# Optimization experiments

Hardware: AMD Instinct MI355X
Metric: run time of the kernel (lower is better)

Reference implementation:

```python
import jax, jax.numpy as jnp
import numpy as np

N = 20000
E = 320000
BS = 1
FG = FN = FE = 128
H = 256


def _mlp_params(key, din, dout):
    dims = [(din, H), (H, H), (H, H), (H, dout)]
    ks = jax.random.split(key, 8)
    ws = [jax.random.normal(ks[2 * i], (a, b), jnp.float32) * (1.0 / np.sqrt(a).astype(np.float32)) for i, (a, b) in enumerate(dims)]
    bs = [jax.random.normal(ks[2 * i + 1], (b,), jnp.float32) * 0.01 for i, (a, b) in enumerate(dims)]
    return ws, bs


def setup_inputs() -> dict:
    key = jax.random.key(0)
    kg, kn, ke, ks, kr, kpe, kpn, kpg = jax.random.split(key, 8)
    inp = {
        'g': jax.random.normal(kg, (BS, FG), jnp.float32),
        'nodes': jax.random.normal(kn, (BS, N, FN), jnp.float32),
        'edges': jax.random.normal(ke, (BS, E, FE), jnp.float32),
        'senders': jax.random.randint(ks, (E,), 0, N, dtype=jnp.int32),
        'receivers': jax.random.randint(kr, (E,), 0, N, dtype=jnp.int32),
    }
    for prefix, kk, din, dout in [('e', kpe, FG + 2 * FN + FE, FE), ('n', kpn, FG + FN + FE, FN), ('g', kpg, FG + FN + FE, FG)]:
        ws, bs = _mlp_params(kk, din, dout)
        for i in range(4):
            inp[f'{prefix}w{i + 1}'] = ws[i]
            inp[f'{prefix}b{i + 1}'] = bs[i]
    return inp


def _mlp(x, w1, b1, w2, b2, w3, b3, w4, b4):
    h = jax.nn.relu(x @ w1 + b1)
    h = jax.nn.relu(h @ w2 + b2)
    h = jax.nn.relu(h @ w3 + b3)
    return h @ w4 + b4


def reference(g, nodes, edges, senders, receivers,
              ew1, eb1, ew2, eb2, ew3, eb3, ew4, eb4,
              nw1, nb1, nw2, nb2, nw3, nb3, nw4, nb4,
              gw1, gb1, gw2, gb2, gw3, gb3, gw4, gb4):
    bs, n_nodes, _ = nodes.shape
    n_edges = edges.shape[1]
    # edge update: concat(g, n_sender, n_receiver, e) -> 4-layer MLP
    g_e = jnp.broadcast_to(g[:, None, :], (bs, n_edges, g.shape[-1]))
    ns = nodes[:, senders]   # [bs, E, FN] gather
    nr = nodes[:, receivers]
    e_new = _mlp(jnp.concatenate([g_e, ns, nr, edges], axis=-1), ew1, eb1, ew2, eb2, ew3, eb3, ew4, eb4)
    # node update: sum of incoming (receiver-indexed) edge feats, scatter-add
    agg = jax.vmap(lambda e: jax.ops.segment_sum(e, receivers, num_segments=n_nodes))(e_new)  # [bs, N, FE]
    g_n = jnp.broadcast_to(g[:, None, :], (bs, n_nodes, g.shape[-1]))
    n_new = _mlp(jnp.concatenate([g_n, nodes, agg], axis=-1), nw1, nb1, nw2, nb2, nw3, nb3, nw4, nb4)
    # graph update: global sums of updated edge and node feats
    e_sum = e_new.sum(axis=1)  # [bs, FE]
    n_sum = n_new.sum(axis=1)  # [bs, FN]
    g_new = _mlp(jnp.concatenate([g, n_sum, e_sum], axis=-1), gw1, gb1, gw2, gb2, gw3, gb3, gw4, gb4)
    return e_new, n_new, g_new
```

## Files before the change

kernel.cpp:

```cpp
#include <hip/hip_runtime.h>
#include <stdint.h>

typedef __attribute__((ext_vector_type(8))) short bf16x8;
typedef __attribute__((ext_vector_type(4))) float f32x4;

#define NE 320000
#define NNODES 20000
#define SMEM_BYTES (65536 + 16384 + 32768)

__device__ __forceinline__ unsigned short f2bf(float f) {
  union { float f; unsigned int u; } v; v.f = f;
  unsigned int u = v.u;
  u += 0x7fffu + ((u >> 16) & 1u);
  return (unsigned short)(u >> 16);
}

__device__ __forceinline__ void gload_lds16(const void* g, void* l) {
  __builtin_amdgcn_global_load_lds((const __attribute__((address_space(1))) void*)g,
                                   (__attribute__((address_space(3))) void*)l, 16, 0, 0);
}

__device__ __forceinline__ void stage_b(const unsigned short* gsrc, char* lds, int nbytes,
                                        int w, int lane) {
  const char* gp = (const char*)gsrc + lane * 16;
  int niss = nbytes >> 10;
#pragma unroll
  for (int i = 0; i < 4; ++i) {
    int idx = w + i * 8;
    if (idx < niss) gload_lds16(gp + (idx << 10), lds + (idx << 10));
  }
}

struct PackArgs {
  const float* src[8];
  unsigned short* dst[8];
  int K[8];
  int N[8];
};

__global__ void pack_weights(PackArgs a) {
  int m = blockIdx.y;
  int K = a.K[m], N = a.N[m];
  int total = (K >> 3) * N;
  int idx = blockIdx.x * 256 + threadIdx.x;
  if (idx >= total) return;
  int n = idx % N;
  int kg = idx / N;
  const float* s = a.src[m];
  bf16x8 p;
#pragma unroll
  for (int j = 0; j < 8; ++j)
    p[j] = (short)f2bf(s[(size_t)(kg * 8 + j) * N + n]);
  *(bf16x8*)(a.dst[m] + (size_t)idx * 8) = p;
}

template <int NB>
__device__ __forceinline__ void compute_chunk(const char* Ab, int rowstride, int kbyte0,
                                              const char* Bb, int NN, int colbase,
                                              int wm, int lhi, int llo, f32x4 (&acc)[2][8]) {
#pragma unroll
  for (int ks = 0; ks < 2; ++ks) {
    bf16x8 a[2];
#pragma unroll
    for (int m = 0; m < 2; ++m) {
      int row = wm * 32 + m * 16 + llo;
      int off = (row * rowstride + kbyte0 + ks * 64 + lhi * 16) ^ ((row & 7) << 4);
      a[m] = *(const bf16x8*)(Ab + off);
    }
    bf16x8 b[NB];
#pragma unroll
    for (int n = 0; n < NB; ++n) {
      int off = ((ks * 4 + lhi) * NN + colbase + n * 16 + llo) * 16;
      b[n] = *(const bf16x8*)(Bb + off);
    }
#pragma unroll
    for (int m = 0; m < 2; ++m)
#pragma unroll
      for (int n = 0; n < NB; ++n)
        acc[m][n] = __builtin_amdgcn_mfma_f32_16x16x32_bf16(a[m], b[n], acc[m][n], 0, 0, 0);
  }
}

__device__ __forceinline__ void zero_acc(f32x4 (&acc)[2][8]) {
  f32x4 z = {0.f, 0.f, 0.f, 0.f};
#pragma unroll
  for (int m = 0; m < 2; ++m)
#pragma unroll
    for (int n = 0; n < 8; ++n) acc[m][n] = z;
}

__device__ __forceinline__ void write_h(char* Hb, const f32x4 (&acc)[2][8], const float* bias,
                                        int wm, int wn, int lhi, int llo) {
#pragma unroll
  for (int n = 0; n < 8; ++n) {
    int col = wn * 128 + n * 16 + llo;
    float bv = bias[col];
#pragma unroll
    for (int m = 0; m < 2; ++m)
#pragma unroll
      for (int q = 0; q < 4; ++q) {
        int row = wm * 32 + m * 16 + lhi * 4 + q;
        float v = fmaxf(acc[m][n][q] + bv, 0.0f);
        int off = (row * 512 + col * 2) ^ ((row & 7) << 4);
        *(unsigned short*)(Hb + off) = f2bf(v);
      }
  }
}

template <int MODE>
__global__ __launch_bounds__(512, 2) void fused_mlp(
    const float* __restrict__ gvec, const float* __restrict__ nodes,
    const float* __restrict__ third, const int* __restrict__ senders,
    const int* __restrict__ receivers,
    const unsigned short* __restrict__ pw1, const unsigned short* __restrict__ pw2,
    const unsigned short* __restrict__ pw3, const unsigned short* __restrict__ pw4,
    const float* __restrict__ b1, const float* __restrict__ b2,
    const float* __restrict__ b3, const float* __restrict__ b4,
    float* __restrict__ outp, float* __restrict__ aggp, float* __restrict__ colsum) {
  constexpr int K1 = (MODE == 0) ? 512 : 384;
  constexpr int KC1 = K1 / 64;
  constexpr int NROWS = (MODE == 0) ? NE : NNODES;

  extern __shared__ char smem[];
  char* Hb = smem;
  char* Ab = smem + 65536;
  char* Bb = smem + 81920;

  const int tid = threadIdx.x;
  const int lane = tid & 63;
  const int w = tid >> 6;
  const int wm = w & 3, wn = w >> 2;
  const int lhi = lane >> 4, llo = lane & 15;
  const int row0 = blockIdx.x * 128;

  const int grow = tid >> 2;
  const int qq = tid & 3;
  const float* src0 = gvec;
  const float* src1;
  const float* src2;
  const float* src3;
  if (MODE == 0) {
    int e = row0 + grow;
    src1 = nodes + (size_t)senders[e] * 128;
    src2 = nodes + (size_t)receivers[e] * 128;
    src3 = third + (size_t)e * 128;
  } else {
    int i = row0 + grow;
    bool v = i < NROWS;
    src1 = v ? nodes + (size_t)i * 128 : gvec;
    src2 = v ? third + (size_t)i * 128 : gvec;
    src3 = gvec;
  }

  f32x4 acc[2][8];
  zero_acc(acc);

  for (int c = 0; c < KC1; ++c) {
    {
      int gc = c * 64 + qq * 16;
      int region = gc >> 7;
      const float* sp = (region == 0) ? src0 : (region == 1) ? src1 : (region == 2) ? src2 : src3;
      sp += (gc & 127);
      f32x4 v0 = *(const f32x4*)(sp);
      f32x4 v1 = *(const f32x4*)(sp + 4);
      f32x4 v2 = *(const f32x4*)(sp + 8);
      f32x4 v3 = *(const f32x4*)(sp + 12);
      bf16x8 p0, p1;
#pragma unroll
      for (int j = 0; j < 4; ++j) {
        p0[j] = (short)f2bf(v0[j]);
        p0[4 + j] = (short)f2bf(v1[j]);
        p1[j] = (short)f2bf(v2[j]);
        p1[4 + j] = (short)f2bf(v3[j]);
      }
      int ab = grow * 128 + qq * 32;
      int sw = (grow & 7) << 4;
      *(bf16x8*)(Ab + (ab ^ sw)) = p0;
      *(bf16x8*)(Ab + ((ab + 16) ^ sw)) = p1;
    }
    stage_b(pw1 + (size_t)c * 16384, Bb, 32768, w, lane);
    __syncthreads();
    compute_chunk<8>(Ab, 128, 0, Bb, 256, wn * 128, wm, lhi, llo, acc);
    __syncthreads();
  }
  write_h(Hb, acc, b1, wm, wn, lhi, llo);
  __syncthreads();

  zero_acc(acc);
  for (int c = 0; c < 4; ++c) {
    stage_b(pw2 + (size_t)c * 16384, Bb, 32768, w, lane);
    __syncthreads();
    compute_chunk<8>(Hb, 512, c * 128, Bb, 256, wn * 128, wm, lhi, llo, acc);
    __syncthreads();
  }
  write_h(Hb, acc, b2, wm, wn, lhi, llo);
  __syncthreads();

  zero_acc(acc);
  for (int c = 0; c < 4; ++c) {
    stage_b(pw3 + (size_t)c * 16384, Bb, 32768, w, lane);
    __syncthreads();
    compute_chunk<8>(Hb, 512, c * 128, Bb, 256, wn * 128, wm, lhi, llo, acc);
    __syncthreads();
  }
  write_h(Hb, acc, b3, wm, wn, lhi, llo);
  __syncthreads();

  zero_acc(acc);
  for (int c = 0; c < 4; ++c) {
    stage_b(pw4 + (size_t)c * 8192, Bb, 16384, w, lane);
    __syncthreads();
    compute_chunk<4>(Hb, 512, c * 128, Bb, 128, wn * 64, wm, lhi, llo, acc);
    __syncthreads();
  }

  float cs[4] = {0.f, 0.f, 0.f, 0.f};
#pragma unroll
  for (int n = 0; n < 4; ++n) {
    int col = wn * 64 + n * 16 + llo;
    float bv = b4[col];
#pragma unroll
    for (int m = 0; m < 2; ++m)
#pragma unroll
      for (int q = 0; q < 4; ++q) {
        int gr = row0 + wm * 32 + m * 16 + lhi * 4 + q;
        float v = acc[m][n][q] + bv;
        if (MODE == 0) {
          outp[(size_t)gr * 128 + col] = v;
          atomicAdd(aggp + (size_t)receivers[gr] * 128 + col, v);
          cs[n] += v;
        } else {
          if (gr < NROWS) {
            outp[(size_t)gr * 128 + col] = v;
            cs[n] += v;
          }
        }
      }
  }
#pragma unroll
  for (int n = 0; n < 4; ++n) {
    float v = cs[n];
    v += __shfl_xor(v, 16);
    v += __shfl_xor(v, 32);
    if (lane < 16) atomicAdd(colsum + wn * 64 + n * 16 + llo, v);
  }
}

__global__ void global_mlp(const float* __restrict__ g, const float* __restrict__ nsum,
                           const float* __restrict__ esum, const float* __restrict__ w1,
                           const float* __restrict__ bb1, const float* __restrict__ w2,
                           const float* __restrict__ bb2, const float* __restrict__ w3,
                           const float* __restrict__ bb3, const float* __restrict__ w4,
                           const float* __restrict__ bb4, float* __restrict__ outg) {
  __shared__ float x[384], h1[256], h2[256], h3[256];
  int t = threadIdx.x;
  if (t < 128) x[t] = g[t];
  else if (t < 256) x[t] = nsum[t - 128];
  else x[t] = esum[t - 256];
  __syncthreads();
  if (t < 256) {
    float a = bb1[t];
    for (int k = 0; k < 384; ++k) a = fmaf(x[k], w1[k * 256 + t], a);
    h1[t] = fmaxf(a, 0.f);
  }
  __syncthreads();
  if (t < 256) {
    float a = bb2[t];
    for (int k = 0; k < 256; ++k) a = fmaf(h1[k], w2[k * 256 + t], a);
    h2[t] = fmaxf(a, 0.f);
  }
  __syncthreads();
  if (t < 256) {
    float a = bb3[t];
    for (int k = 0; k < 256; ++k) a = fmaf(h2[k], w3[k * 256 + t], a);
    h3[t] = fmaxf(a, 0.f);
  }
  __syncthreads();
  if (t < 128) {
    float a = bb4[t];
    for (int k = 0; k < 256; ++k) a = fmaf(h3[k], w4[k * 128 + t], a);
    outg[t] = a;
  }
}

extern "C" void kernel_launch(void* const* d_in, const int* in_sizes, int n_in, void* d_out,
                              int out_size, void* d_ws, size_t ws_size, hipStream_t stream) {
  const float* g = (const float*)d_in[0];
  const float* nodes = (const float*)d_in[1];
  const float* edges = (const float*)d_in[2];
  const int* senders = (const int*)d_in[3];
  const int* receivers = (const int*)d_in[4];
  const float* ew[4] = {(const float*)d_in[5], (const float*)d_in[7], (const float*)d_in[9],
                        (const float*)d_in[11]};
  const float* eb[4] = {(const float*)d_in[6], (const float*)d_in[8], (const float*)d_in[10],
                        (const float*)d_in[12]};
  const float* nw[4] = {(const float*)d_in[13], (const float*)d_in[15], (const float*)d_in[17],
                        (const float*)d_in[19]};
  const float* nb[4] = {(const float*)d_in[14], (const float*)d_in[16], (const float*)d_in[18],
                        (const float*)d_in[20]};
  const float* gw[4] = {(const float*)d_in[21], (const float*)d_in[23], (const float*)d_in[25],
                        (const float*)d_in[27]};
  const float* gb[4] = {(const float*)d_in[22], (const float*)d_in[24], (const float*)d_in[26],
                        (const float*)d_in[28]};

  float* out = (float*)d_out;
  float* e_new = out;
  float* n_new = out + (size_t)NE * 128;
  float* g_new = n_new + (size_t)NNODES * 128;

  char* ws = (char*)d_ws;
  unsigned short* pe1 = (unsigned short*)ws;
  unsigned short* pe2 = pe1 + 512 * 256;
  unsigned short* pe3 = pe2 + 256 * 256;
  unsigned short* pe4 = pe3 + 256 * 256;
  unsigned short* pn1 = pe4 + 256 * 128;
  unsigned short* pn2 = pn1 + 384 * 256;
  unsigned short* pn3 = pn2 + 256 * 256;
  unsigned short* pn4 = pn3 + 256 * 256;
  float* agg = (float*)(ws + 1114112);
  float* esum = agg + (size_t)NNODES * 128;
  float* nsum = esum + 128;

  hipMemsetAsync(agg, 0, (size_t)NNODES * 128 * 4 + 1024, stream);

  PackArgs pa;
  const float* srcs[8] = {ew[0], ew[1], ew[2], ew[3], nw[0], nw[1], nw[2], nw[3]};
  unsigned short* dsts[8] = {pe1, pe2, pe3, pe4, pn1, pn2, pn3, pn4};
  int Ks[8] = {512, 256, 256, 256, 384, 256, 256, 256};
  int Ns[8] = {256, 256, 256, 128, 256, 256, 256, 128};
  for (int i = 0; i < 8; ++i) {
    pa.src[i] = srcs[i];
    pa.dst[i] = dsts[i];
    pa.K[i] = Ks[i];
    pa.N[i] = Ns[i];
  }
  pack_weights<<<dim3(64, 8), 256, 0, stream>>>(pa);

  hipFuncSetAttribute((const void*)&fused_mlp<0>, hipFuncAttributeMaxDynamicSharedMemorySize,
                      SMEM_BYTES);
  hipFuncSetAttribute((const void*)&fused_mlp<1>, hipFuncAttributeMaxDynamicSharedMemorySize,
                      SMEM_BYTES);

  fused_mlp<0><<<NE / 128, 512, SMEM_BYTES, stream>>>(
      g, nodes, edges, senders, receivers, pe1, pe2, pe3, pe4, eb[0], eb[1], eb[2], eb[3], e_new,
      agg, esum);
  fused_mlp<1><<<(NNODES + 127) / 128, 512, SMEM_BYTES, stream>>>(
      g, nodes, agg, senders, receivers, pn1, pn2, pn3, pn4, nb[0], nb[1], nb[2], nb[3], n_new,
      nullptr, nsum);
  global_mlp<<<1, 384, 0, stream>>>(g, nsum, esum, gw[0], gb[0], gw[1], gb[1], gw[2], gb[2], gw[3],
                                    gb[3], g_new);
}
```

Baseline: 587.6 us.

## Double-buffer A and weight tiles in LDS and prefetch across MLP layers

Splits the A-operand and weight-staging LDS buffers into ping-pong pairs. The next chunk's gathered inputs and weight tile are loaded while the current chunk computes, and the first weight tile of the following layer is prefetched during the last chunk of the current one. This drops one barrier per chunk and is meant to hide global-load latency behind MFMA work. In exchange, LDS per block grows to 160KB and the launch-bounds hint for two blocks per CU is removed, so occupancy likely falls to one 512-thread block per CU.

```diff
diff --git a/kernel.cpp b/kernel.cpp
--- a/kernel.cpp
+++ b/kernel.cpp
@@ -6,7 +6,7 @@
 
 #define NE 320000
 #define NNODES 20000
-#define SMEM_BYTES (65536 + 16384 + 32768)
+#define SMEM_BYTES 163840
 
 __device__ __forceinline__ unsigned short f2bf(float f) {
   union { float f; unsigned int u; } v; v.f = f;
@@ -107,8 +107,34 @@
   }
 }
 
+__device__ __forceinline__ void gather_regs(int gc, const float* src0, const float* src1,
+                                            const float* src2, const float* src3, f32x4 (&v)[4]) {
+  int region = gc >> 7;
+  const float* sp = (region == 0) ? src0 : (region == 1) ? src1 : (region == 2) ? src2 : src3;
+  sp += (gc & 127);
+  v[0] = *(const f32x4*)(sp);
+  v[1] = *(const f32x4*)(sp + 4);
+  v[2] = *(const f32x4*)(sp + 8);
+  v[3] = *(const f32x4*)(sp + 12);
+}
+
+__device__ __forceinline__ void pack_write_A(char* Abuf, int grow, int qq, const f32x4 (&v)[4]) {
+  bf16x8 p0, p1;
+#pragma unroll
+  for (int j = 0; j < 4; ++j) {
+    p0[j] = (short)f2bf(v[0][j]);
+    p0[4 + j] = (short)f2bf(v[1][j]);
+    p1[j] = (short)f2bf(v[2][j]);
+    p1[4 + j] = (short)f2bf(v[3][j]);
+  }
+  int ab = grow * 128 + qq * 32;
+  int sw = (grow & 7) << 4;
+  *(bf16x8*)(Abuf + (ab ^ sw)) = p0;
+  *(bf16x8*)(Abuf + ((ab + 16) ^ sw)) = p1;
+}
+
 template <int MODE>
-__global__ __launch_bounds__(512, 2) void fused_mlp(
+__global__ __launch_bounds__(512) void fused_mlp(
     const float* __restrict__ gvec, const float* __restrict__ nodes,
     const float* __restrict__ third, const int* __restrict__ senders,
     const int* __restrict__ receivers,
@@ -123,8 +149,10 @@
 
   extern __shared__ char smem[];
   char* Hb = smem;
-  char* Ab = smem + 65536;
-  char* Bb = smem + 81920;
+  char* Ab0 = smem + 65536;
+  char* Ab1 = smem + 81920;
+  char* Bb0 = smem + 98304;
+  char* Bb1 = smem + 131072;
 
   const int tid = threadIdx.x;
   const int lane = tid & 63;
@@ -155,62 +183,61 @@
   f32x4 acc[2][8];
   zero_acc(acc);
 
+  {
+    f32x4 v[4];
+    gather_regs(qq * 16, src0, src1, src2, src3, v);
+    pack_write_A(Ab0, grow, qq, v);
+  }
+  stage_b(pw1, Bb0, 32768, w, lane);
+  __syncthreads();
+
+#pragma unroll
   for (int c = 0; c < KC1; ++c) {
-    {
-      int gc = c * 64 + qq * 16;
-      int region = gc >> 7;
-      const float* sp = (region == 0) ? src0 : (region == 1) ? src1 : (region == 2) ? src2 : src3;
-      sp += (gc & 127);
-      f32x4 v0 = *(const f32x4*)(sp);
-      f32x4 v1 = *(const f32x4*)(sp + 4);
-      f32x4 v2 = *(const f32x4*)(sp + 8);
-      f32x4 v3 = *(const f32x4*)(sp + 12);
-      bf16x8 p0, p1;
-#pragma unroll
-      for (int j = 0; j < 4; ++j) {
-        p0[j] = (short)f2bf(v0[j]);
-        p0[4 + j] = (short)f2bf(v1[j]);
-        p1[j] = (short)f2bf(v2[j]);
-        p1[4 + j] = (short)f2bf(v3[j]);
-      }
-      int ab = grow * 128 + qq * 32;
-      int sw = (grow & 7) << 4;
-      *(bf16x8*)(Ab + (ab ^ sw)) = p0;
-      *(bf16x8*)(Ab + ((ab + 16) ^ sw)) = p1;
+    char* Bn = ((c + 1) & 1) ? Bb1 : Bb0;
+    f32x4 v[4];
+    if (c + 1 < KC1) {
+      gather_regs((c + 1) * 64 + qq * 16, src0, src1, src2, src3, v);
+      stage_b(pw1 + (size_t)(c + 1) * 16384, Bn, 32768, w, lane);
+    } else {
+      stage_b(pw2, Bn, 32768, w, lane);
     }
-    stage_b(pw1 + (size_t)c * 16384, Bb, 32768, w, lane);
+    compute_chunk<8>((c & 1) ? Ab1 : Ab0, 128, 0, (c & 1) ? Bb1 : Bb0, 256, wn * 128, wm, lhi,
+                     llo, acc);
+    if (c + 1 < KC1) pack_write_A(((c + 1) & 1) ? Ab1 : Ab0, grow, qq, v);
     __syncthreads();
-    compute_chunk<8>(Ab, 128, 0, Bb, 256, wn * 128, wm, lhi, llo, acc);
+  }
+  write_h(Hb, acc, b1, wm, wn, lhi, llo);
+  __syncthreads();
+
+  zero_acc(acc);
+#pragma unroll
+  for (int c = 0; c < 4; ++c) {
+    char* Bn = ((c + 1) & 1) ? Bb1 : Bb0;
+    if (c < 3) stage_b(pw2 + (size_t)(c + 1) * 16384, Bn, 32768, w, lane);
+    else stage_b(pw3, Bn, 32768, w, lane);
+    compute_chunk<8>(Hb, 512, c * 128, (c & 1) ? Bb1 : Bb0, 256, wn * 128, wm, lhi, llo, acc);
     __syncthreads();
   }
-  write_h(Hb, acc, b1, wm, wn, lhi, llo);
+  write_h(Hb, acc, b2, wm, wn, lhi, llo);
   __syncthreads();
 
   zero_acc(acc);
+#pragma unroll
   for (int c = 0; c < 4; ++c) {
-    stage_b(pw2 + (size_t)c * 16384, Bb, 32768, w, lane);
+    char* Bn = ((c + 1) & 1) ? Bb1 : Bb0;
+    if (c < 3) stage_b(pw3 + (size_t)(c + 1) * 16384, Bn, 32768, w, lane);
+    else stage_b(pw4, Bn, 16384, w, lane);
+    compute_chunk<8>(Hb, 512, c * 128, (c & 1) ? Bb1 : Bb0, 256, wn * 128, wm, lhi, llo, acc);
     __syncthreads();
-    compute_chunk<8>(Hb, 512, c * 128, Bb, 256, wn * 128, wm, lhi, llo, acc);
-    __syncthreads();
-  }
-  write_h(Hb, acc, b2, wm, wn, lhi, llo);
+  }
+  write_h(Hb, acc, b3, wm, wn, lhi, llo);
   __syncthreads();
 
   zero_acc(acc);
+#pragma unroll
   for (int c = 0; c < 4; ++c) {
-    stage_b(pw3 + (size_t)c * 16384, Bb, 32768, w, lane);
-    __syncthreads();
-    compute_chunk<8>(Hb, 512, c * 128, Bb, 256, wn * 128, wm, lhi, llo, acc);
-    __syncthreads();
-  }
-  write_h(Hb, acc, b3, wm, wn, lhi, llo);
-  __syncthreads();
-
-  zero_acc(acc);
-  for (int c = 0; c < 4; ++c) {
-    stage_b(pw4 + (size_t)c * 8192, Bb, 16384, w, lane);
-    __syncthreads();
-    compute_chunk<4>(Hb, 512, c * 128, Bb, 128, wn * 64, wm, lhi, llo, acc);
+    if (c < 3) stage_b(pw4 + (size_t)(c + 1) * 8192, ((c + 1) & 1) ? Bb1 : Bb0, 16384, w, lane);
+    compute_chunk<4>(Hb, 512, c * 128, (c & 1) ? Bb1 : Bb0, 128, wn * 64, wm, lhi, llo, acc);
     __syncthreads();
   }
 
```

Result: faster. 556.6 us (-5.3%).
